# Kernel tuning notes

Hardware: AMD Instinct MI355X
Metric: run time of the kernel (lower is better)

The kernel has to match this reference:

```python
import jax, jax.numpy as jnp
import numpy as np

D_IN = 64      # num_in_features
D_OUT = 64     # num_out_features
H = 512        # neurons_per_layer
M = 64         # num_meta_in_features
META_OUT = D_IN * H + H + H * D_OUT + D_OUT  # 66112
B = 2048


def setup_inputs() -> dict:
    key = jax.random.key(0)
    k1, k2, k3 = jax.random.split(key, 3)
    x = jax.random.normal(k1, (B, D_IN + M), dtype=jnp.float32)
    # xavier-normal-ish init for the two hypernet linears, zero biases
    W_in = jax.random.normal(k2, (H, M), dtype=jnp.float32) * jnp.sqrt(2.0 / (H + M))
    b_in = jnp.zeros((H,), dtype=jnp.float32)
    W_out = jax.random.normal(k3, (META_OUT, H), dtype=jnp.float32) * jnp.sqrt(2.0 / (META_OUT + H))
    b_out = jnp.zeros((META_OUT,), dtype=jnp.float32)
    return {"x": x, "W_in": W_in, "b_in": b_in, "W_out": W_out, "b_out": b_out}


def reference(x, W_in, b_in, W_out, b_out):
    real = x[:, :D_IN]            # [B, D_IN]
    meta = x[:, D_IN:]            # [B, M]
    h = jax.nn.elu(meta @ W_in.T + b_in)          # [B, H]
    gen = h @ W_out.T + b_out                     # [B, META_OUT]
    base = D_IN * H
    l_in_w = gen[:, :base].reshape(-1, D_IN, H)   # [B, D_IN, H]
    l_in_b = gen[:, base:base + H]                # [B, H]
    base += H
    add = H * D_OUT
    l_out_w = gen[:, base:base + add].reshape(-1, H, D_OUT)  # [B, H, D_OUT]
    l_out_b = gen[:, base + add:]                 # [B, D_OUT]
    # tensordot(real, l_in_w, dims=([1],[1])).diagonal(0,1).T == per-sample matvec
    y = jax.nn.elu(jnp.einsum('bi,bih->bh', real, l_in_w) + l_in_b)
    out = jnp.einsum('bh,bho->bo', y, l_out_w) + l_out_b
    return out
```

## Files before the change

kernel.cpp:

```cpp
#include <hip/hip_runtime.h>
#include <hip/hip_bf16.h>
#include <stdint.h>

#define B_N   2048
#define XW    128
#define KDIM  512
#define NROWS_W   66112
#define NROWS_PAD 66560

typedef __bf16 v8bf  __attribute__((ext_vector_type(8)));
typedef float  f32x4 __attribute__((ext_vector_type(4)));

__device__ __forceinline__ unsigned short f2bf(float f) {
    uint32_t u = __float_as_uint(f);
    u += 0x7FFF + ((u >> 16) & 1);
    return (unsigned short)(u >> 16);
}
__device__ __forceinline__ float elu1(float v) {
    return v > 0.0f ? v : expm1f(v);
}
__device__ __forceinline__ void gload_lds16(const void* g, void* l) {
    __builtin_amdgcn_global_load_lds(
        (const __attribute__((address_space(1))) unsigned int*)g,
        (__attribute__((address_space(3))) unsigned int*)l, 16, 0, 0);
}

__global__ void k_h(const float* __restrict__ x, const float* __restrict__ W_in,
                    const float* __restrict__ b_in, unsigned short* __restrict__ hb) {
    int idx = blockIdx.x * 256 + threadIdx.x;
    int b = idx >> 9, j = idx & 511;
    const float4* xm = (const float4*)(x + (size_t)b * XW + 64);
    const float4* wr = (const float4*)(W_in + (size_t)j * 64);
    float acc = 0.f;
#pragma unroll
    for (int q = 0; q < 16; ++q) {
        float4 a = xm[q], w = wr[q];
        acc += a.x * w.x + a.y * w.y + a.z * w.z + a.w * w.w;
    }
    acc = elu1(acc + b_in[j]);
    hb[idx] = f2bf(acc);
}

__global__ void k_conv(const float* __restrict__ Wf, unsigned short* __restrict__ Wb) {
    size_t c = (size_t)blockIdx.x * 256 + threadIdx.x;
    size_t row = c >> 6; int kk = (int)(c & 63);
    union { uint4 v; unsigned short u[8]; } o;
    o.v = (uint4){0, 0, 0, 0};
    if (row < NROWS_W) {
        const float* wp = Wf + row * KDIM + kk * 8;
        float4 w0 = *(const float4*)wp, w1 = *(const float4*)(wp + 4);
        o.u[0] = f2bf(w0.x); o.u[1] = f2bf(w0.y); o.u[2] = f2bf(w0.z); o.u[3] = f2bf(w0.w);
        o.u[4] = f2bf(w1.x); o.u[5] = f2bf(w1.y); o.u[6] = f2bf(w1.z); o.u[7] = f2bf(w1.w);
    }
    *(uint4*)(Wb + c * 8) = o.v;
}

__global__ void k_init_ypre(const float* __restrict__ x, const float* __restrict__ b_out,
                            float* __restrict__ ypre) {
    int idx = blockIdx.x * 256 + threadIdx.x;
    int b = idx >> 9, hh = idx & 511;
    float acc = b_out[32768 + hh];
    const float* xr = x + (size_t)b * XW;
#pragma unroll 8
    for (int i = 0; i < 64; ++i)
        acc += xr[i] * b_out[i * 512 + hh];
    ypre[idx] = acc;
}

__global__ void k_y(const float* __restrict__ ypre, float* __restrict__ yv) {
    int idx = blockIdx.x * 256 + threadIdx.x;
    yv[idx] = elu1(ypre[idx]);
}

__global__ void k_init_out(const float* __restrict__ yv, const float* __restrict__ b_out,
                           float* __restrict__ out) {
    int idx = blockIdx.x * 256 + threadIdx.x;
    int b = idx >> 6, o = idx & 63;
    float acc = b_out[66048 + o];
    const float* yr = yv + (size_t)b * 512;
#pragma unroll 4
    for (int hh = 0; hh < 512; ++hh)
        acc += yr[hh] * b_out[33280 + hh * 64 + o];
    out[idx] = acc;
}

template<int MODE>
__global__ __launch_bounds__(256, 2)
void k_pgemm(const unsigned short* __restrict__ hb,
             const unsigned short* __restrict__ Wb,
             const float* __restrict__ scaleSrc,
             float* __restrict__ outAcc) {
    constexpr int NP   = MODE ? 129 : 130;
    constexpr int OUTW = MODE ? 64 : 512;
    constexpr int SCW  = MODE ? 18 : 9;

    __shared__ char smem[3 * 16384 + SCW * 128 * 4];
    char* Bs = smem;
    float* sc = (float*)(smem + 3 * 16384);

    const int lid = blockIdx.x;
    const int s   = (lid & 7) * 2 + (lid >> 8);
    const int inner = (lid >> 3) & 31;
    const int m0  = (inner & 15) * 128;
    const int nh  = inner >> 4;

    const int pBeg = (NP * s) >> 4;
    const int pEnd = (NP * (s + 1)) >> 4;
    const int halfS = (MODE == 0 && pBeg >= 65) ? 1 : 0;
    const int iBeg  = pBeg - halfS * 65;

    const int tid = threadIdx.x;
    const int wid = tid >> 6, l = tid & 63;
    const int lr = l & 15, lg = l >> 4;
    const int wm = wid >> 1, wn = wid & 1;

    for (int c = tid; c < SCW * 128; c += 256) {
        int jj = c >> 7, row = c & 127;
        float v = 1.0f;
        if (MODE == 0) {
            int i = iBeg + jj;
            if (i < 64) v = scaleSrc[(size_t)(m0 + row) * XW + i];
        } else {
            int g = (pBeg + (jj >> 1)) * 4 + nh * 2 + (jj & 1);
            if (g < 512) v = scaleSrc[(size_t)(m0 + row) * KDIM + g];
        }
        sc[c] = v;
    }
    __syncthreads();

    int bB[4], bX[4];
#pragma unroll
    for (int q = 0; q < 4; ++q) {
        int rb = wn * 64 + q * 16 + lr;
        bB[q] = rb * 128; bX[q] = rb & 7;
    }

    f32x4 accP[4][4], accO[4][4];
#pragma unroll
    for (int mi = 0; mi < 4; ++mi)
#pragma unroll
        for (int ni = 0; ni < 4; ++ni) {
            accP[mi][ni] = (f32x4){0.f, 0.f, 0.f, 0.f};
            accO[mi][ni] = (f32x4){0.f, 0.f, 0.f, 0.f};
        }

    for (int kq = 0; kq < 4; ++kq) {
        auto stageB = [&](int slot, int t) {
            int p = pBeg + (t >> 1), k0c = t & 1;
            int wrow = MODE ? (33280 + p * 256 + nh * 128)
                            : ((p - halfS * 65) * 512 + halfS * 256 + nh * 128);
            const int rsub = tid >> 3;
            const int sl = (tid & 7) ^ (rsub & 7);
            const unsigned short* src0 = Wb + (size_t)(wrow + rsub) * KDIM
                                       + kq * 128 + k0c * 64 + sl * 8;
            char* dst0 = Bs + slot * 16384 + tid * 16;
#pragma unroll
            for (int q = 0; q < 4; ++q)
                gload_lds16(src0 + (size_t)q * 32 * KDIM, dst0 + q * 4096);
        };

        const unsigned short* abase = hb + (size_t)(m0 + wm * 64 + lr) * KDIM
                                    + kq * 128 + lg * 8;
        v8bf areg[4][4];
#pragma unroll
        for (int mi = 0; mi < 4; ++mi)
#pragma unroll
            for (int kk2 = 0; kk2 < 4; ++kk2)
                areg[mi][kk2] = *(const v8bf*)(abase + mi * 16 * KDIM + kk2 * 32);

        const int NPH = 2 * (pEnd - pBeg);
        stageB(0, 0);
        stageB(1, 1);
        int slc = 0;

        for (int p = pBeg; p < pEnd; ++p) {
#pragma unroll
            for (int k0 = 0; k0 < 2; ++k0) {
                const int t = (p - pBeg) * 2 + k0;
                int ns = slc + 2; if (ns >= 3) ns -= 3;
                if (t + 2 < NPH) {
                    stageB(ns, t + 2);
                    asm volatile("s_waitcnt vmcnt(8)" ::: "memory");
                } else if (t + 1 < NPH) {
                    asm volatile("s_waitcnt vmcnt(4)" ::: "memory");
                } else {
                    asm volatile("s_waitcnt vmcnt(0)" ::: "memory");
                }
                __builtin_amdgcn_s_barrier();
                asm volatile("" ::: "memory");
                char* Bbuf = Bs + slc * 16384;
                __builtin_amdgcn_s_setprio(1);
#pragma unroll
                for (int ks = 0; ks < 2; ++ks) {
                    v8bf bfr[4];
                    const int sB = ks * 4 + lg;
#pragma unroll
                    for (int ni = 0; ni < 4; ++ni)
                        bfr[ni] = *(const v8bf*)(Bbuf + bB[ni] + ((sB ^ bX[ni]) << 4));
#pragma unroll
                    for (int mi = 0; mi < 4; ++mi)
#pragma unroll
                        for (int ni = 0; ni < 4; ++ni)
                            accP[mi][ni] = __builtin_amdgcn_mfma_f32_16x16x32_bf16(
                                areg[mi][k0 * 2 + ks], bfr[ni], accP[mi][ni], 0, 0, 0);
                }
                __builtin_amdgcn_s_setprio(0);
                if (k0 == 1) {
                    const int pp = p - pBeg;
                    const int jj = MODE ? (pp * 2 + wn) : pp;
                    const f32x4* scv = (const f32x4*)(sc + jj * 128);
#pragma unroll
                    for (int mi = 0; mi < 4; ++mi) {
                        f32x4 sv = scv[wm * 16 + mi * 4 + lg];
#pragma unroll
                        for (int ni = 0; ni < 4; ++ni) {
                            accO[mi][ni] += sv * accP[mi][ni];
                            accP[mi][ni] = (f32x4){0.f, 0.f, 0.f, 0.f};
                        }
                    }
                }
                asm volatile("" ::: "memory");
                __builtin_amdgcn_s_barrier();
                slc = (slc == 2) ? 0 : slc + 1;
            }
        }
    }
#pragma unroll
    for (int mi = 0; mi < 4; ++mi)
#pragma unroll
        for (int ni = 0; ni < 4; ++ni)
#pragma unroll
            for (int r = 0; r < 4; ++r) {
                int row = wm * 64 + mi * 16 + lg * 4 + r;
                int col = MODE ? (ni * 16 + lr)
                               : (halfS * 256 + nh * 128 + wn * 64 + ni * 16 + lr);
                atomicAdd(outAcc + (size_t)(m0 + row) * OUTW + col, accO[mi][ni][r]);
            }
}

extern "C" void kernel_launch(void* const* d_in, const int* in_sizes, int n_in,
                              void* d_out, int out_size, void* d_ws, size_t ws_size,
                              hipStream_t stream) {
    const float* x     = (const float*)d_in[0];
    const float* W_in  = (const float*)d_in[1];
    const float* b_in  = (const float*)d_in[2];
    const float* W_out = (const float*)d_in[3];
    const float* b_out = (const float*)d_in[4];
    float* out = (float*)d_out;

    char* ws = (char*)d_ws;
    unsigned short* hb = (unsigned short*)ws;
    float* ypre        = (float*)(ws + (2u << 20));
    float* yv          = (float*)(ws + (6u << 20));
    unsigned short* Wb = (unsigned short*)(ws + (10u << 20));

    k_h<<<(B_N * 512) / 256, 256, 0, stream>>>(x, W_in, b_in, hb);
    k_conv<<<(NROWS_PAD * KDIM / 8) / 256, 256, 0, stream>>>(W_out, Wb);

    k_init_ypre<<<(B_N * 512) / 256, 256, 0, stream>>>(x, b_out, ypre);

    k_pgemm<0><<<512, 256, 0, stream>>>(hb, Wb, x, ypre);

    k_y<<<(B_N * 512) / 256, 256, 0, stream>>>(ypre, yv);

    k_init_out<<<(B_N * 64) / 256, 256, 0, stream>>>(yv, b_out, out);

    k_pgemm<1><<<512, 256, 0, stream>>>(hb, Wb, yv, out);
}
```

Baseline: 292.9 us.

## Load B fragments directly from global into registers, drop LDS pipeline

```diff
diff --git a/kernel.cpp b/kernel.cpp
--- a/kernel.cpp
+++ b/kernel.cpp
@@ -18,11 +18,6 @@
 }
 __device__ __forceinline__ float elu1(float v) {
     return v > 0.0f ? v : expm1f(v);
-}
-__device__ __forceinline__ void gload_lds16(const void* g, void* l) {
-    __builtin_amdgcn_global_load_lds(
-        (const __attribute__((address_space(1))) unsigned int*)g,
-        (__attribute__((address_space(3))) unsigned int*)l, 16, 0, 0);
 }
 
 __global__ void k_h(const float* __restrict__ x, const float* __restrict__ W_in,
@@ -94,15 +89,13 @@
     constexpr int OUTW = MODE ? 64 : 512;
     constexpr int SCW  = MODE ? 18 : 9;
 
-    __shared__ char smem[3 * 16384 + SCW * 128 * 4];
-    char* Bs = smem;
-    float* sc = (float*)(smem + 3 * 16384);
+    __shared__ float sc[SCW * 128];
 
     const int lid = blockIdx.x;
-    const int s   = (lid & 7) * 2 + (lid >> 8);
-    const int inner = (lid >> 3) & 31;
-    const int m0  = (inner & 15) * 128;
-    const int nh  = inner >> 4;
+    const int c8 = lid & 7, u = (lid >> 3) & 15, v = lid >> 7;
+    const int combo = c8 + 8 * v;
+    const int s  = combo >> 1, nh = combo & 1;
+    const int m0 = u * 128;
 
     const int pBeg = (NP * s) >> 4;
     const int pEnd = (NP * (s + 1)) >> 4;
@@ -116,24 +109,17 @@
 
     for (int c = tid; c < SCW * 128; c += 256) {
         int jj = c >> 7, row = c & 127;
-        float v = 1.0f;
+        float vs = 1.0f;
         if (MODE == 0) {
             int i = iBeg + jj;
-            if (i < 64) v = scaleSrc[(size_t)(m0 + row) * XW + i];
+            if (i < 64) vs = scaleSrc[(size_t)(m0 + row) * XW + i];
         } else {
             int g = (pBeg + (jj >> 1)) * 4 + nh * 2 + (jj & 1);
-            if (g < 512) v = scaleSrc[(size_t)(m0 + row) * KDIM + g];
+            if (g < 512) vs = scaleSrc[(size_t)(m0 + row) * KDIM + g];
         }
-        sc[c] = v;
+        sc[c] = vs;
     }
     __syncthreads();
-
-    int bB[4], bX[4];
-#pragma unroll
-    for (int q = 0; q < 4; ++q) {
-        int rb = wn * 64 + q * 16 + lr;
-        bB[q] = rb * 128; bX[q] = rb & 7;
-    }
 
     f32x4 accP[4][4], accO[4][4];
 #pragma unroll
@@ -145,20 +131,6 @@
         }
 
     for (int kq = 0; kq < 4; ++kq) {
-        auto stageB = [&](int slot, int t) {
-            int p = pBeg + (t >> 1), k0c = t & 1;
-            int wrow = MODE ? (33280 + p * 256 + nh * 128)
-                            : ((p - halfS * 65) * 512 + halfS * 256 + nh * 128);
-            const int rsub = tid >> 3;
-            const int sl = (tid & 7) ^ (rsub & 7);
-            const unsigned short* src0 = Wb + (size_t)(wrow + rsub) * KDIM
-                                       + kq * 128 + k0c * 64 + sl * 8;
-            char* dst0 = Bs + slot * 16384 + tid * 16;
-#pragma unroll
-            for (int q = 0; q < 4; ++q)
-                gload_lds16(src0 + (size_t)q * 32 * KDIM, dst0 + q * 4096);
-        };
-
         const unsigned short* abase = hb + (size_t)(m0 + wm * 64 + lr) * KDIM
                                     + kq * 128 + lg * 8;
         v8bf areg[4][4];
@@ -168,60 +140,59 @@
             for (int kk2 = 0; kk2 < 4; ++kk2)
                 areg[mi][kk2] = *(const v8bf*)(abase + mi * 16 * KDIM + kk2 * 32);
 
-        const int NPH = 2 * (pEnd - pBeg);
-        stageB(0, 0);
-        stageB(1, 1);
-        int slc = 0;
-
         for (int p = pBeg; p < pEnd; ++p) {
-#pragma unroll
-            for (int k0 = 0; k0 < 2; ++k0) {
-                const int t = (p - pBeg) * 2 + k0;
-                int ns = slc + 2; if (ns >= 3) ns -= 3;
-                if (t + 2 < NPH) {
-                    stageB(ns, t + 2);
-                    asm volatile("s_waitcnt vmcnt(8)" ::: "memory");
-                } else if (t + 1 < NPH) {
-                    asm volatile("s_waitcnt vmcnt(4)" ::: "memory");
-                } else {
-                    asm volatile("s_waitcnt vmcnt(0)" ::: "memory");
-                }
-                __builtin_amdgcn_s_barrier();
-                asm volatile("" ::: "memory");
-                char* Bbuf = Bs + slc * 16384;
-                __builtin_amdgcn_s_setprio(1);
-#pragma unroll
-                for (int ks = 0; ks < 2; ++ks) {
-                    v8bf bfr[4];
-                    const int sB = ks * 4 + lg;
-#pragma unroll
-                    for (int ni = 0; ni < 4; ++ni)
-                        bfr[ni] = *(const v8bf*)(Bbuf + bB[ni] + ((sB ^ bX[ni]) << 4));
-#pragma unroll
-                    for (int mi = 0; mi < 4; ++mi)
-#pragma unroll
-                        for (int ni = 0; ni < 4; ++ni)
-                            accP[mi][ni] = __builtin_amdgcn_mfma_f32_16x16x32_bf16(
-                                areg[mi][k0 * 2 + ks], bfr[ni], accP[mi][ni], 0, 0, 0);
-                }
-                __builtin_amdgcn_s_setprio(0);
-                if (k0 == 1) {
-                    const int pp = p - pBeg;
-                    const int jj = MODE ? (pp * 2 + wn) : pp;
-                    const f32x4* scv = (const f32x4*)(sc + jj * 128);
-#pragma unroll
-                    for (int mi = 0; mi < 4; ++mi) {
-                        f32x4 sv = scv[wm * 16 + mi * 4 + lg];
-#pragma unroll
-                        for (int ni = 0; ni < 4; ++ni) {
-                            accO[mi][ni] += sv * accP[mi][ni];
-                            accP[mi][ni] = (f32x4){0.f, 0.f, 0.f, 0.f};
-                        }
+            const int wrow = MODE ? (33280 + p * 256 + nh * 128)
+                                  : ((p - halfS * 65) * 512 + halfS * 256 + nh * 128);
+            const unsigned short* bbase = Wb + (size_t)(wrow + wn * 64 + lr) * KDIM
+                                        + kq * 128 + lg * 8;
+            v8bf b0[4], b1[4], b2[4], b3[4];
+#pragma unroll
+            for (int ni = 0; ni < 4; ++ni) b0[ni] = *(const v8bf*)(bbase + ni * 16 * KDIM);
+#pragma unroll
+            for (int ni = 0; ni < 4; ++ni) b1[ni] = *(const v8bf*)(bbase + ni * 16 * KDIM + 32);
+#pragma unroll
+            for (int ni = 0; ni < 4; ++ni) b2[ni] = *(const v8bf*)(bbase + ni * 16 * KDIM + 64);
+#pragma unroll
+            for (int ni = 0; ni < 4; ++ni) b3[ni] = *(const v8bf*)(bbase + ni * 16 * KDIM + 96);
+            __builtin_amdgcn_s_setprio(1);
+#pragma unroll
+            for (int mi = 0; mi < 4; ++mi)
+#pragma unroll
+                for (int ni = 0; ni < 4; ++ni)
+                    accP[mi][ni] = __builtin_amdgcn_mfma_f32_16x16x32_bf16(
+                        areg[mi][0], b0[ni], accP[mi][ni], 0, 0, 0);
+#pragma unroll
+            for (int mi = 0; mi < 4; ++mi)
+#pragma unroll
+                for (int ni = 0; ni < 4; ++ni)
+                    accP[mi][ni] = __builtin_amdgcn_mfma_f32_16x16x32_bf16(
+                        areg[mi][1], b1[ni], accP[mi][ni], 0, 0, 0);
+#pragma unroll
+            for (int mi = 0; mi < 4; ++mi)
+#pragma unroll
+                for (int ni = 0; ni < 4; ++ni)
+                    accP[mi][ni] = __builtin_amdgcn_mfma_f32_16x16x32_bf16(
+                        areg[mi][2], b2[ni], accP[mi][ni], 0, 0, 0);
+#pragma unroll
+            for (int mi = 0; mi < 4; ++mi)
+#pragma unroll
+                for (int ni = 0; ni < 4; ++ni)
+                    accP[mi][ni] = __builtin_amdgcn_mfma_f32_16x16x32_bf16(
+                        areg[mi][3], b3[ni], accP[mi][ni], 0, 0, 0);
+            __builtin_amdgcn_s_setprio(0);
+            {
+                const int pp = p - pBeg;
+                const int jj = MODE ? (pp * 2 + wn) : pp;
+                const f32x4* scv = (const f32x4*)(sc + jj * 128);
+#pragma unroll
+                for (int mi = 0; mi < 4; ++mi) {
+                    f32x4 sv = scv[wm * 16 + mi * 4 + lg];
+#pragma unroll
+                    for (int ni = 0; ni < 4; ++ni) {
+                        accO[mi][ni] += sv * accP[mi][ni];
+                        accP[mi][ni] = (f32x4){0.f, 0.f, 0.f, 0.f};
                     }
                 }
-                asm volatile("" ::: "memory");
-                __builtin_amdgcn_s_barrier();
-                slc = (slc == 2) ? 0 : slc + 1;
             }
         }
     }
```

New measurement: 419.1 us. +43.1%, slower.
